# Performance work log

Hardware: AMD Instinct MI355X
Metric: run time of the kernel (lower is better)

## Reference

```python
import jax, jax.numpy as jnp
import numpy as np

B, S, D, H = 4, 2048, 1024, 16
HD = D // H
ROPE_THETA = 10000.0


def setup_inputs() -> dict:
    key = jax.random.key(0)
    ks = jax.random.split(key, 5)
    scale = 1.0 / np.sqrt(D)
    inp = {
        "x": jax.random.normal(ks[0], (B, S, D), dtype=jnp.float32),
        "Wq": jax.random.normal(ks[1], (D, D), dtype=jnp.float32) * scale,
        "bq": jnp.zeros((D,), jnp.float32),
        "Wk": jax.random.normal(ks[2], (D, D), dtype=jnp.float32) * scale,
        "bk": jnp.zeros((D,), jnp.float32),
        "Wv": jax.random.normal(ks[3], (D, D), dtype=jnp.float32) * scale,
        "bv": jnp.zeros((D,), jnp.float32),
        "Wo": jax.random.normal(ks[4], (D, D), dtype=jnp.float32) * scale,
        "bo": jnp.zeros((D,), jnp.float32),
        # causal mask: True means masked (j > i), matching masked_fill semantics
        "attn_mask": jnp.triu(jnp.ones((S, S), dtype=bool), k=1),
    }
    return inp


def _rope(x):
    # x: [B, H, S, HD]; half-split rotary embedding
    half = HD // 2
    inv_freq = 1.0 / (ROPE_THETA ** (jnp.arange(0, half, dtype=jnp.float32) / half))
    pos = jnp.arange(x.shape[2], dtype=jnp.float32)
    freqs = pos[:, None] * inv_freq[None, :]            # [S, half]
    cos = jnp.cos(freqs)[None, None]                    # [1,1,S,half]
    sin = jnp.sin(freqs)[None, None]
    x1, x2 = x[..., :half], x[..., half:]
    return jnp.concatenate([x1 * cos - x2 * sin, x2 * cos + x1 * sin], axis=-1)


def reference(x, Wq, bq, Wk, bk, Wv, bv, Wo, bo, attn_mask):
    def shape(t):  # [B,S,D] -> [B,H,S,HD]
        return t.reshape(B, S, H, HD).transpose(0, 2, 1, 3)

    q = shape(x @ Wq.T + bq)
    k = shape(x @ Wk.T + bk)
    v = shape(x @ Wv.T + bv)
    q = _rope(q)
    k = _rope(k)
    scores = jnp.einsum("bhqd,bhkd->bhqk", q, k) * (HD ** -0.5)
    scores = jnp.where(attn_mask[None, None], -jnp.inf, scores)
    w = jax.nn.softmax(scores, axis=-1)
    attn = jnp.einsum("bhqk,bhkd->bhqd", w, v)
    merged = attn.transpose(0, 2, 1, 3).reshape(B, S, D)
    return merged @ Wo.T + bo
```

## Files before the change

### kernel.cpp

```cpp
#include <hip/hip_runtime.h>
#include <math.h>

#define BATCH 4
#define SEQ   2048
#define DMODEL 1024
#define NHEAD 16
#define HDIM  64
#define MROWS (BATCH*SEQ)

typedef unsigned short u16;
typedef unsigned int   u32;

using bf16x8 = __attribute__((ext_vector_type(8))) short;
using f32x4  = __attribute__((ext_vector_type(4))) float;
using f32x16 = __attribute__((ext_vector_type(16))) float;

__device__ __forceinline__ u16 f2bf(float f) {
    u32 u = __float_as_uint(f);
    u += 0x7fffu + ((u >> 16) & 1u);
    return (u16)(u >> 16);
}
__device__ __forceinline__ u32 pack2bf(float a, float b) {
    u32 ua = __float_as_uint(a); ua += 0x7fffu + ((ua >> 16) & 1u);
    u32 ub = __float_as_uint(b); ub += 0x7fffu + ((ub >> 16) & 1u);
    return (ua >> 16) | (ub & 0xffff0000u);
}

#define GLOBAL_LOAD_LDS16(gp, lp)                                              \
    __builtin_amdgcn_global_load_lds(                                          \
        (const __attribute__((address_space(1))) void*)(gp),                   \
        (__attribute__((address_space(3))) void*)(lp), 16, 0, 0)

__global__ __launch_bounds__(256) void convert_inputs(
    const float* __restrict__ x,  const float* __restrict__ wq,
    const float* __restrict__ wk, const float* __restrict__ wv,
    const float* __restrict__ wo, u16* __restrict__ dst)
{
    long long i4 = ((long long)blockIdx.x * 256 + threadIdx.x) * 4;
    const float* src; long long off;
    if (i4 < 8388608LL) { src = x; off = i4; }
    else {
        long long j = i4 - 8388608LL;
        int seg = (int)(j >> 20);
        off = j & 1048575LL;
        src = (seg == 0) ? wq : (seg == 1) ? wk : (seg == 2) ? wv : wo;
    }
    float4 v = *(const float4*)(src + off);
    u32 lo = (u32)f2bf(v.x) | ((u32)f2bf(v.y) << 16);
    u32 hi = (u32)f2bf(v.z) | ((u32)f2bf(v.w) << 16);
    *(uint2*)(dst + i4) = make_uint2(lo, hi);
}

template<int QKV>
__global__ __launch_bounds__(256) void gemm_mfma(
    const u16* __restrict__ A,
    const u16* __restrict__ Wq_, const u16* __restrict__ Wk_, const u16* __restrict__ Wv_,
    const float* __restrict__ bq_, const float* __restrict__ bk_, const float* __restrict__ bv_,
    u16* __restrict__ Cq_, u16* __restrict__ Ck_, u16* __restrict__ Cv_,
    float* __restrict__ Cf)
{
    __shared__ u16 As[128 * 32];
    __shared__ u16 Ws[128 * 32];

    const int t    = threadIdx.x;
    const int lane = t & 63;
    const int w    = t >> 6;
    const int quad = lane >> 4;
    const int l15  = lane & 15;

    const int bx  = blockIdx.x;
    const int xcd = bx & 7;
    const int i_  = bx >> 3;
    const int bml = i_ & 7;
    const int n_  = (QKV ? ((i_ >> 3) & 7) : (i_ >> 3));
    const int seg = (QKV ? (i_ >> 6) : 0);

    const u16*   W    = (seg == 0) ? Wq_ : (seg == 1) ? Wk_ : Wv_;
    const float* bias = (seg == 0) ? bq_ : (seg == 1) ? bk_ : bv_;
    u16*         Cb   = (seg == 0) ? Cq_ : (seg == 1) ? Ck_ : Cv_;

    const int bm   = (xcd * 8 + bml) * 128;
    const int bn   = n_ * 128;
    const int wrow = (w & 1) * 64;
    const int wcol = (w >> 1) * 64;

    const int srl = lane >> 2;
    const int sc  = (lane & 3) ^ ((lane >> 3) & 3);

    f32x4 acc[4][4] = {};

    for (int k0 = 0; k0 < DMODEL; k0 += 32) {
        __syncthreads();
        #pragma unroll
        for (int i = 0; i < 2; i++) {
            int row = 32 * w + 16 * i + srl;
            GLOBAL_LOAD_LDS16(A + (size_t)(bm + row) * DMODEL + k0 + sc * 8,
                              &As[(32 * w + 16 * i) * 32]);
            GLOBAL_LOAD_LDS16(W + (size_t)(bn + row) * DMODEL + k0 + sc * 8,
                              &Ws[(32 * w + 16 * i) * 32]);
        }
        __syncthreads();

        bf16x8 af[4], bfr[4];
        const int pc = quad ^ ((l15 >> 1) & 3);
        #pragma unroll
        for (int i = 0; i < 4; i++)
            af[i] = *(const bf16x8*)&As[(wrow + 16 * i + l15) * 32 + pc * 8];
        #pragma unroll
        for (int j = 0; j < 4; j++)
            bfr[j] = *(const bf16x8*)&Ws[(wcol + 16 * j + l15) * 32 + pc * 8];
        #pragma unroll
        for (int i = 0; i < 4; i++)
            #pragma unroll
            for (int j = 0; j < 4; j++)
                acc[i][j] = __builtin_amdgcn_mfma_f32_16x16x32_bf16(af[i], bfr[j], acc[i][j], 0, 0, 0);
    }

    float bv[4];
    #pragma unroll
    for (int j = 0; j < 4; j++) bv[j] = bias[bn + wcol + 16 * j + l15];

    if constexpr (QKV == 0) {
        #pragma unroll
        for (int i = 0; i < 4; i++)
            #pragma unroll
            for (int r = 0; r < 4; r++) {
                int mg = bm + wrow + 16 * i + quad * 4 + r;
                #pragma unroll
                for (int j = 0; j < 4; j++)
                    Cf[(size_t)mg * DMODEL + bn + wcol + 16 * j + l15] = acc[i][j][r] + bv[j];
            }
    } else {
        if (seg == 2) {
            #pragma unroll
            for (int i = 0; i < 4; i++)
                #pragma unroll
                for (int r = 0; r < 4; r++) {
                    int mg = bm + wrow + 16 * i + quad * 4 + r;
                    #pragma unroll
                    for (int j = 0; j < 4; j++)
                        Cb[(size_t)mg * DMODEL + bn + wcol + 16 * j + l15] = f2bf(acc[i][j][r] + bv[j]);
                }
        } else {
            const float qscale = (seg == 0) ? 0.125f : 1.0f;
            float inv[2];
            #pragma unroll
            for (int j = 0; j < 2; j++) {
                int d = 16 * j + l15;
                inv[j] = exp2f(-(float)d * 0.4152410118609203f);
            }
            #pragma unroll
            for (int i = 0; i < 4; i++)
                #pragma unroll
                for (int r = 0; r < 4; r++) {
                    int mg = bm + wrow + 16 * i + quad * 4 + r;
                    int s  = mg & (SEQ - 1);
                    #pragma unroll
                    for (int j = 0; j < 2; j++) {
                        float f = (float)s * inv[j];
                        float sn, cs;
                        __sincosf(f, &sn, &cs);
                        float a1 = acc[i][j][r]     + bv[j];
                        float a2 = acc[i][j + 2][r] + bv[j + 2];
                        float o1 = (a1 * cs - a2 * sn) * qscale;
                        float o2 = (a2 * cs + a1 * sn) * qscale;
                        Cb[(size_t)mg * DMODEL + bn + wcol + 16 * j       + l15] = f2bf(o1);
                        Cb[(size_t)mg * DMODEL + bn + wcol + 16 * (j + 2) + l15] = f2bf(o2);
                    }
                }
        }
    }
}

__global__ __launch_bounds__(256) void attn_mfma(
    const u16* __restrict__ Q, const u16* __restrict__ K,
    const u16* __restrict__ V, u16* __restrict__ O)
{
    __shared__ u16 Qs[128 * 64];
    __shared__ u16 Ks[64 * 64];
    __shared__ u16 Vt[64 * 64];
    __shared__ u16 Ps[128 * 64];
    __shared__ float lS[128];

    const int t    = threadIdx.x;
    const int lane = t & 63;
    const int w    = t >> 6;
    const int l31  = lane & 31;
    const int hl   = lane >> 5;
    const int bid  = blockIdx.x;
    const int bh   = bid & 63;
    const int qt   = 15 - (bid >> 6);
    const int h    = bh & (NHEAD - 1);
    const int b    = bh >> 4;
    const int q0   = qt * 128;

    const size_t gbase = ((size_t)b * SEQ) * DMODEL + h * HDIM;

    {
        int rl = lane >> 3, cp = lane & 7;
        int c  = cp ^ rl;
        #pragma unroll
        for (int i = 0; i < 4; i++) {
            int row = 32 * w + 8 * i + rl;
            GLOBAL_LOAD_LDS16(Q + gbase + (size_t)(q0 + row) * DMODEL + c * 8,
                              &Qs[(32 * w + 8 * i) * 64]);
        }
    }
    __syncthreads();

    bf16x8 qf[4];
    {
        int row = 32 * w + l31;
        #pragma unroll
        for (int s = 0; s < 4; s++) {
            int c = (hl + 2 * s) ^ (row & 7);
            qf[s] = *(const bf16x8*)&Qs[row * 64 + c * 8];
        }
    }

    float lsum = 0.0f;
    f32x16 oacc[2] = {};

    const int ktn = 2 * qt + 2;
    for (int kt = 0; kt < ktn; kt++) {
        const int k0 = kt * 64;
        __syncthreads();

        {
            int rl = lane >> 3, cp = lane & 7;
            int c  = cp ^ rl;
            #pragma unroll
            for (int i = 0; i < 2; i++) {
                int row = 16 * w + 8 * i + rl;
                GLOBAL_LOAD_LDS16(K + gbase + (size_t)(k0 + row) * DMODEL + c * 8,
                                  &Ks[(16 * w + 8 * i) * 64]);
            }
        }
        {
            int j0 = (t & 31) * 2, d0 = (t >> 5) * 8;
            uint4 va = *(const uint4*)(V + gbase + (size_t)(k0 + j0)     * DMODEL + d0);
            uint4 vb = *(const uint4*)(V + gbase + (size_t)(k0 + j0 + 1) * DMODEL + d0);
            const u16* pa = (const u16*)&va;
            const u16* pb = (const u16*)&vb;
            int jd = t & 31, pos = jd & 3, ch = jd >> 2;
            #pragma unroll
            for (int e = 0; e < 8; e++) {
                int row = d0 + e;
                int pcch = ch ^ (row & 7);
                *(u32*)&Vt[row * 64 + pcch * 8 + pos * 2] = (u32)pa[e] | ((u32)pb[e] << 16);
            }
        }
        __syncthreads();

        const bool act = (k0 <= q0 + 32 * w + 31);
        if (act) {
            const int qrow = 32 * w + l31;
            const int qg   = q0 + qrow;
            #pragma unroll
            for (int krh = 0; krh < 2; krh++) {
                const bool qact = (k0 + 32 * krh <= q0 + 32 * w + 31);
                if (!qact) {
                    #pragma unroll
                    for (int g = 0; g < 4; g++)
                        #pragma unroll
                        for (int pp = 0; pp < 2; pp++) {
                            int kr = 32 * krh + 8 * g + 4 * hl + 2 * pp;
                            int jd = kr >> 1;
                            int pcc = (jd >> 2) ^ (qrow & 7);
                            *(u32*)&Ps[qrow * 64 + pcc * 8 + (jd & 3) * 2] = 0u;
                        }
                    continue;
                }
                f32x16 s = {};
                #pragma unroll
                for (int stp = 0; stp < 4; stp++) {
                    int row = 32 * krh + l31;
                    int c   = (hl + 2 * stp) ^ (l31 & 7);
                    bf16x8 ka = *(const bf16x8*)&Ks[row * 64 + c * 8];
                    s = __builtin_amdgcn_mfma_f32_32x32x16_bf16(ka, qf[stp], s, 0, 0, 0);
                }
                if (k0 + 32 * krh + 31 > q0 + 32 * w) {
                    #pragma unroll
                    for (int r = 0; r < 16; r++) {
                        int krg = k0 + 32 * krh + (r & 3) + 8 * (r >> 2) + 4 * hl;
                        if (krg > qg) s[r] = -1e30f;
                    }
                }
                float pv[16];
                #pragma unroll
                for (int r = 0; r < 16; r++) { pv[r] = __expf(s[r]); lsum += pv[r]; }
                #pragma unroll
                for (int g = 0; g < 4; g++)
                    #pragma unroll
                    for (int pp = 0; pp < 2; pp++) {
                        int kr = 32 * krh + 8 * g + 4 * hl + 2 * pp;
                        int jd = kr >> 1;
                        int pcc = (jd >> 2) ^ (qrow & 7);
                        *(u32*)&Ps[qrow * 64 + pcc * 8 + (jd & 3) * 2] =
                            pack2bf(pv[4 * g + 2 * pp], pv[4 * g + 2 * pp + 1]);
                    }
            }

            #pragma unroll
            for (int stp = 0; stp < 4; stp++) {
                int c = (hl + 2 * stp) ^ (l31 & 7);
                bf16x8 pf = *(const bf16x8*)&Ps[qrow * 64 + c * 8];
                #pragma unroll
                for (int dh = 0; dh < 2; dh++) {
                    bf16x8 vf = *(const bf16x8*)&Vt[(32 * dh + l31) * 64 + c * 8];
                    oacc[dh] = __builtin_amdgcn_mfma_f32_32x32x16_bf16(pf, vf, oacc[dh], 0, 0, 0);
                }
            }
        }
    }

    lsum += __shfl_xor(lsum, 32, 64);
    if (lane < 32) lS[32 * w + lane] = lsum;
    __syncthreads();

    #pragma unroll
    for (int g = 0; g < 4; g++) {
        f32x4 lv = *(const f32x4*)&lS[32 * w + 8 * g + 4 * hl];
        #pragma unroll
        for (int rr = 0; rr < 4; rr++) {
            int qg = q0 + 32 * w + rr + 8 * g + 4 * hl;
            float inv = 1.0f / lv[rr];
            #pragma unroll
            for (int dh = 0; dh < 2; dh++) {
                float o = oacc[dh][4 * g + rr] * inv;
                O[gbase + (size_t)qg * DMODEL + 32 * dh + l31] = f2bf(o);
            }
        }
    }
}

extern "C" void kernel_launch(void* const* d_in, const int* in_sizes, int n_in,
                              void* d_out, int out_size, void* d_ws, size_t ws_size,
                              hipStream_t stream)
{
    const float* x  = (const float*)d_in[0];
    const float* Wq = (const float*)d_in[1];
    const float* bq = (const float*)d_in[2];
    const float* Wk = (const float*)d_in[3];
    const float* bk = (const float*)d_in[4];
    const float* Wv = (const float*)d_in[5];
    const float* bv = (const float*)d_in[6];
    const float* Wo = (const float*)d_in[7];
    const float* bo = (const float*)d_in[8];

    u16* wsp = (u16*)d_ws;
    u16* xb  = wsp;
    u16* Wqb = wsp + 8388608;
    u16* Wkb = Wqb + 1048576;
    u16* Wvb = Wkb + 1048576;
    u16* Wob = Wvb + 1048576;
    u16* Qb  = Wob + 1048576;
    u16* Kb  = Qb + 8388608;
    u16* Vb  = Kb + 8388608;
    u16* Ab  = Vb + 8388608;

    convert_inputs<<<12288, 256, 0, stream>>>(x, Wq, Wk, Wv, Wo, xb);

    gemm_mfma<1><<<1536, 256, 0, stream>>>(xb, Wqb, Wkb, Wvb, bq, bk, bv,
                                           Qb, Kb, Vb, nullptr);

    attn_mfma<<<1024, 256, 0, stream>>>(Qb, Kb, Vb, Ab);

    gemm_mfma<0><<<512, 256, 0, stream>>>(Ab, Wob, nullptr, nullptr, bo, nullptr, nullptr,
                                          nullptr, nullptr, nullptr, (float*)d_out);
}
```

Baseline: 280.0 us.

## Shrink attention query tile to 64 rows with 2 waves and reuse Q smem for P

The attention kernel now processes 64 query rows per block with 128 threads and launches twice as many blocks. The Q buffer is reused for P after Q fragments are loaded into registers, which cuts shared memory per block. The log2(e) factor is folded into the Q scale so exp2f replaces __expf. Smaller blocks should improve occupancy and load balance over the causal triangle, at the cost of each block loading K/V twice as often per query row.

After: 298.4 us. 6.6% more time.

```diff
diff --git a/kernel.cpp b/kernel.cpp
--- a/kernel.cpp
+++ b/kernel.cpp
@@ -142,7 +142,7 @@
                         Cb[(size_t)mg * DMODEL + bn + wcol + 16 * j + l15] = f2bf(acc[i][j][r] + bv[j]);
                 }
         } else {
-            const float qscale = (seg == 0) ? 0.125f : 1.0f;
+            const float qscale = (seg == 0) ? 0.18033688011112042f : 1.0f;
             float inv[2];
             #pragma unroll
             for (int j = 0; j < 2; j++) {
@@ -172,15 +172,14 @@
     }
 }
 
-__global__ __launch_bounds__(256) void attn_mfma(
+__global__ __launch_bounds__(128) void attn_mfma(
     const u16* __restrict__ Q, const u16* __restrict__ K,
     const u16* __restrict__ V, u16* __restrict__ O)
 {
-    __shared__ u16 Qs[128 * 64];
+    __shared__ u16 QPs[64 * 64];
     __shared__ u16 Ks[64 * 64];
     __shared__ u16 Vt[64 * 64];
-    __shared__ u16 Ps[128 * 64];
-    __shared__ float lS[128];
+    __shared__ float lS[64];
 
     const int t    = threadIdx.x;
     const int lane = t & 63;
@@ -189,10 +188,10 @@
     const int hl   = lane >> 5;
     const int bid  = blockIdx.x;
     const int bh   = bid & 63;
-    const int qt   = 15 - (bid >> 6);
+    const int qt   = 31 - (bid >> 6);
     const int h    = bh & (NHEAD - 1);
     const int b    = bh >> 4;
-    const int q0   = qt * 128;
+    const int q0   = qt * 64;
 
     const size_t gbase = ((size_t)b * SEQ) * DMODEL + h * HDIM;
 
@@ -203,26 +202,24 @@
         for (int i = 0; i < 4; i++) {
             int row = 32 * w + 8 * i + rl;
             GLOBAL_LOAD_LDS16(Q + gbase + (size_t)(q0 + row) * DMODEL + c * 8,
-                              &Qs[(32 * w + 8 * i) * 64]);
+                              &QPs[(32 * w + 8 * i) * 64]);
         }
     }
     __syncthreads();
 
+    const int qrow = 32 * w + l31;
+    const int qg   = q0 + qrow;
     bf16x8 qf[4];
-    {
-        int row = 32 * w + l31;
-        #pragma unroll
-        for (int s = 0; s < 4; s++) {
-            int c = (hl + 2 * s) ^ (row & 7);
-            qf[s] = *(const bf16x8*)&Qs[row * 64 + c * 8];
-        }
+    #pragma unroll
+    for (int s = 0; s < 4; s++) {
+        int c = (hl + 2 * s) ^ (qrow & 7);
+        qf[s] = *(const bf16x8*)&QPs[qrow * 64 + c * 8];
     }
 
     float lsum = 0.0f;
     f32x16 oacc[2] = {};
 
-    const int ktn = 2 * qt + 2;
-    for (int kt = 0; kt < ktn; kt++) {
+    for (int kt = 0; kt <= qt; kt++) {
         const int k0 = kt * 64;
         __syncthreads();
 
@@ -230,92 +227,92 @@
             int rl = lane >> 3, cp = lane & 7;
             int c  = cp ^ rl;
             #pragma unroll
-            for (int i = 0; i < 2; i++) {
-                int row = 16 * w + 8 * i + rl;
+            for (int i = 0; i < 4; i++) {
+                int row = 32 * w + 8 * i + rl;
                 GLOBAL_LOAD_LDS16(K + gbase + (size_t)(k0 + row) * DMODEL + c * 8,
-                                  &Ks[(16 * w + 8 * i) * 64]);
+                                  &Ks[(32 * w + 8 * i) * 64]);
             }
         }
         {
-            int j0 = (t & 31) * 2, d0 = (t >> 5) * 8;
-            uint4 va = *(const uint4*)(V + gbase + (size_t)(k0 + j0)     * DMODEL + d0);
-            uint4 vb = *(const uint4*)(V + gbase + (size_t)(k0 + j0 + 1) * DMODEL + d0);
-            const u16* pa = (const u16*)&va;
-            const u16* pb = (const u16*)&vb;
-            int jd = t & 31, pos = jd & 3, ch = jd >> 2;
-            #pragma unroll
-            for (int e = 0; e < 8; e++) {
-                int row = d0 + e;
-                int pcch = ch ^ (row & 7);
-                *(u32*)&Vt[row * 64 + pcch * 8 + pos * 2] = (u32)pa[e] | ((u32)pb[e] << 16);
+            int u = t >> 2, v = t & 3;
+            int j0 = 2 * u;
+            #pragma unroll
+            for (int half = 0; half < 2; half++) {
+                int ch = v + 4 * half;
+                int d0 = ch * 8;
+                uint4 va = *(const uint4*)(V + gbase + (size_t)(k0 + j0)     * DMODEL + d0);
+                uint4 vb = *(const uint4*)(V + gbase + (size_t)(k0 + j0 + 1) * DMODEL + d0);
+                const u16* pa = (const u16*)&va;
+                const u16* pb = (const u16*)&vb;
+                int pos = u & 3, kch = u >> 2;
+                #pragma unroll
+                for (int e = 0; e < 8; e++) {
+                    int row  = d0 + e;
+                    int pcch = kch ^ (row & 7);
+                    *(u32*)&Vt[row * 64 + pcch * 8 + pos * 2] = (u32)pa[e] | ((u32)pb[e] << 16);
+                }
             }
         }
         __syncthreads();
 
-        const bool act = (k0 <= q0 + 32 * w + 31);
-        if (act) {
-            const int qrow = 32 * w + l31;
-            const int qg   = q0 + qrow;
-            #pragma unroll
-            for (int krh = 0; krh < 2; krh++) {
-                const bool qact = (k0 + 32 * krh <= q0 + 32 * w + 31);
-                if (!qact) {
-                    #pragma unroll
-                    for (int g = 0; g < 4; g++)
-                        #pragma unroll
-                        for (int pp = 0; pp < 2; pp++) {
-                            int kr = 32 * krh + 8 * g + 4 * hl + 2 * pp;
-                            int jd = kr >> 1;
-                            int pcc = (jd >> 2) ^ (qrow & 7);
-                            *(u32*)&Ps[qrow * 64 + pcc * 8 + (jd & 3) * 2] = 0u;
-                        }
-                    continue;
-                }
-                f32x16 s = {};
-                #pragma unroll
-                for (int stp = 0; stp < 4; stp++) {
-                    int row = 32 * krh + l31;
-                    int c   = (hl + 2 * stp) ^ (l31 & 7);
-                    bf16x8 ka = *(const bf16x8*)&Ks[row * 64 + c * 8];
-                    s = __builtin_amdgcn_mfma_f32_32x32x16_bf16(ka, qf[stp], s, 0, 0, 0);
-                }
-                if (k0 + 32 * krh + 31 > q0 + 32 * w) {
-                    #pragma unroll
-                    for (int r = 0; r < 16; r++) {
-                        int krg = k0 + 32 * krh + (r & 3) + 8 * (r >> 2) + 4 * hl;
-                        if (krg > qg) s[r] = -1e30f;
-                    }
-                }
-                float pv[16];
-                #pragma unroll
-                for (int r = 0; r < 16; r++) { pv[r] = __expf(s[r]); lsum += pv[r]; }
+        const bool diagt = (kt == qt);
+        #pragma unroll
+        for (int krh = 0; krh < 2; krh++) {
+            if (diagt && krh > w) {
                 #pragma unroll
                 for (int g = 0; g < 4; g++)
                     #pragma unroll
                     for (int pp = 0; pp < 2; pp++) {
-                        int kr = 32 * krh + 8 * g + 4 * hl + 2 * pp;
-                        int jd = kr >> 1;
+                        int jd  = 16 * krh + 4 * g + 2 * hl + pp;
                         int pcc = (jd >> 2) ^ (qrow & 7);
-                        *(u32*)&Ps[qrow * 64 + pcc * 8 + (jd & 3) * 2] =
-                            pack2bf(pv[4 * g + 2 * pp], pv[4 * g + 2 * pp + 1]);
+                        *(u32*)&QPs[qrow * 64 + pcc * 8 + (jd & 3) * 2] = 0u;
                     }
-            }
-
+                continue;
+            }
+            f32x16 s = {};
             #pragma unroll
             for (int stp = 0; stp < 4; stp++) {
-                int c = (hl + 2 * stp) ^ (l31 & 7);
-                bf16x8 pf = *(const bf16x8*)&Ps[qrow * 64 + c * 8];
-                #pragma unroll
-                for (int dh = 0; dh < 2; dh++) {
-                    bf16x8 vf = *(const bf16x8*)&Vt[(32 * dh + l31) * 64 + c * 8];
-                    oacc[dh] = __builtin_amdgcn_mfma_f32_32x32x16_bf16(pf, vf, oacc[dh], 0, 0, 0);
-                }
+                int row = 32 * krh + l31;
+                int c   = (hl + 2 * stp) ^ (row & 7);
+                bf16x8 ka = *(const bf16x8*)&Ks[row * 64 + c * 8];
+                s = __builtin_amdgcn_mfma_f32_32x32x16_bf16(ka, qf[stp], s, 0, 0, 0);
+            }
+            if (diagt && krh == w) {
+                #pragma unroll
+                for (int r = 0; r < 16; r++) {
+                    int krg = k0 + 32 * krh + (r & 3) + 8 * (r >> 2) + 4 * hl;
+                    if (krg > qg) s[r] = -1e30f;
+                }
+            }
+            float pv[16];
+            #pragma unroll
+            for (int r = 0; r < 16; r++) { pv[r] = exp2f(s[r]); lsum += pv[r]; }
+            #pragma unroll
+            for (int g = 0; g < 4; g++)
+                #pragma unroll
+                for (int pp = 0; pp < 2; pp++) {
+                    int jd  = 16 * krh + 4 * g + 2 * hl + pp;
+                    int pcc = (jd >> 2) ^ (qrow & 7);
+                    *(u32*)&QPs[qrow * 64 + pcc * 8 + (jd & 3) * 2] =
+                        pack2bf(pv[4 * g + 2 * pp], pv[4 * g + 2 * pp + 1]);
+                }
+        }
+
+        #pragma unroll
+        for (int stp = 0; stp < 4; stp++) {
+            int c = (hl + 2 * stp) ^ (qrow & 7);
+            bf16x8 pf = *(const bf16x8*)&QPs[qrow * 64 + c * 8];
+            #pragma unroll
+            for (int dh = 0; dh < 2; dh++) {
+                int vr = 32 * dh + l31;
+                bf16x8 vf = *(const bf16x8*)&Vt[vr * 64 + ((hl + 2 * stp) ^ (vr & 7)) * 8];
+                oacc[dh] = __builtin_amdgcn_mfma_f32_32x32x16_bf16(pf, vf, oacc[dh], 0, 0, 0);
             }
         }
     }
 
     lsum += __shfl_xor(lsum, 32, 64);
-    if (lane < 32) lS[32 * w + lane] = lsum;
+    if (hl == 0) lS[32 * w + l31] = lsum;
     __syncthreads();
 
     #pragma unroll
@@ -323,12 +320,12 @@
         f32x4 lv = *(const f32x4*)&lS[32 * w + 8 * g + 4 * hl];
         #pragma unroll
         for (int rr = 0; rr < 4; rr++) {
-            int qg = q0 + 32 * w + rr + 8 * g + 4 * hl;
+            int qgw = q0 + 32 * w + rr + 8 * g + 4 * hl;
             float inv = 1.0f / lv[rr];
             #pragma unroll
             for (int dh = 0; dh < 2; dh++) {
                 float o = oacc[dh][4 * g + rr] * inv;
-                O[gbase + (size_t)qg * DMODEL + 32 * dh + l31] = f2bf(o);
+                O[gbase + (size_t)qgw * DMODEL + 32 * dh + l31] = f2bf(o);
             }
         }
     }
@@ -364,7 +361,7 @@
     gemm_mfma<1><<<1536, 256, 0, stream>>>(xb, Wqb, Wkb, Wvb, bq, bk, bv,
                                            Qb, Kb, Vb, nullptr);
 
-    attn_mfma<<<1024, 256, 0, stream>>>(Qb, Kb, Vb, Ab);
+    attn_mfma<<<2048, 128, 0, stream>>>(Qb, Kb, Vb, Ab);
 
     gemm_mfma<0><<<512, 256, 0, stream>>>(Ab, Wob, nullptr, nullptr, bo, nullptr, nullptr,
                                           nullptr, nullptr, nullptr, (float*)d_out);
```
